# Kernel tuning notes

Measured on AMD Instinct MI355X. Metric: run time of the kernel, lower is better.

The kernel has to match this reference:

```python
import jax, jax.numpy as jnp
import numpy as np

B, S, D, H, DFF = 4, 2048, 768, 12, 3072
DK = D // H

def setup_inputs() -> dict:
    key = jax.random.key(0)
    ks = jax.random.split(key, 16)
    sc = 0.02
    inp = {
        'src': jax.random.normal(ks[0], (B, S, D), jnp.float32),
        'mask': jnp.ones((B, 1, 1, S), jnp.int32),
        'Wq': jax.random.normal(ks[1], (D, D), jnp.float32) * sc,
        'bq': jnp.zeros((D,), jnp.float32),
        'Wk': jax.random.normal(ks[2], (D, D), jnp.float32) * sc,
        'bk': jnp.zeros((D,), jnp.float32),
        'Wv': jax.random.normal(ks[3], (D, D), jnp.float32) * sc,
        'bv': jnp.zeros((D,), jnp.float32),
        'Wo': jax.random.normal(ks[4], (D, D), jnp.float32) * sc,
        'bo': jnp.zeros((D,), jnp.float32),
        'W1': jax.random.normal(ks[5], (D, DFF), jnp.float32) * sc,
        'b1': jnp.zeros((DFF,), jnp.float32),
        'W2': jax.random.normal(ks[6], (DFF, D), jnp.float32) * sc,
        'b2': jnp.zeros((D,), jnp.float32),
        'ln1_g': jnp.ones((D,), jnp.float32), 'ln1_b': jnp.zeros((D,), jnp.float32),
        'ln2_g': jnp.ones((D,), jnp.float32), 'ln2_b': jnp.zeros((D,), jnp.float32),
    }
    return inp

def _layernorm(x, g, b, eps=1e-5):
    mu = jnp.mean(x, axis=-1, keepdims=True)
    var = jnp.mean(jnp.square(x - mu), axis=-1, keepdims=True)
    return (x - mu) * jax.lax.rsqrt(var + eps) * g + b

def reference(src, mask, Wq, bq, Wk, bk, Wv, bv, Wo, bo, W1, b1, W2, b2, ln1_g, ln1_b, ln2_g, ln2_b):
    # Multi-head self-attention (dropout in eval mode -> identity)
    q = (src @ Wq + bq).reshape(B, S, H, DK).transpose(0, 2, 1, 3)  # [B,H,S,dk]
    k = (src @ Wk + bk).reshape(B, S, H, DK).transpose(0, 2, 1, 3)
    v = (src @ Wv + bv).reshape(B, S, H, DK).transpose(0, 2, 1, 3)
    scores = jnp.einsum('bhqd,bhkd->bhqk', q, k) / jnp.sqrt(jnp.float32(DK))
    scores = jnp.where(mask == 0, jnp.float32(-1e9), scores)
    attn = jax.nn.softmax(scores, axis=-1)
    ctx = jnp.einsum('bhqk,bhkd->bhqd', attn, v)  # [B,H,S,dk]
    ctx = ctx.transpose(0, 2, 1, 3).reshape(B, S, D)
    attn_out = ctx @ Wo + bo
    x = _layernorm(src + attn_out, ln1_g, ln1_b)
    ffn = jax.nn.relu(x @ W1 + b1) @ W2 + b2
    return _layernorm(x + ffn, ln2_g, ln2_b)
```

## Files before the change

kernel.cpp:

```cpp
#include <hip/hip_runtime.h>
#include <hip/hip_bf16.h>
#include <stdint.h>

constexpr int BB = 4;
constexpr int SS = 2048;
constexpr int DD = 768;
constexpr int HH = 12;
constexpr int DKK = 64;
constexpr int DFF2 = 3072;
constexpr int MR = BB * SS;

typedef __attribute__((ext_vector_type(4))) short short4v;
typedef __attribute__((ext_vector_type(8))) short short8v;
typedef __attribute__((ext_vector_type(4))) float f32x4;
typedef __attribute__((ext_vector_type(16))) float f32x16;
typedef __attribute__((ext_vector_type(4))) float float4v;
typedef __attribute__((ext_vector_type(4))) unsigned int u32x4;

static __device__ inline short f2bs(float f) {
    __hip_bfloat16 h = __float2bfloat16(f);
    return (short)__builtin_bit_cast(unsigned short, h);
}
static __device__ inline float bs2f(short s) {
    __hip_bfloat16 h = __builtin_bit_cast(__hip_bfloat16, (unsigned short)s);
    return __bfloat162float(h);
}

static __device__ inline void glds16(const void* g, void* l) {
    __builtin_amdgcn_global_load_lds(
        (const __attribute__((address_space(1))) void*)g,
        (__attribute__((address_space(3))) void*)l, 16, 0, 0);
}

static __device__ inline unsigned cvtpk(float a, float b) {
    unsigned d;
    asm("v_cvt_pk_bf16_f32 %0, %1, %2" : "=v"(d) : "v"(a), "v"(b));
    return d;
}
static __device__ inline short8v pk4(unsigned a, unsigned b, unsigned c, unsigned d) {
    u32x4 w; w[0] = a; w[1] = b; w[2] = c; w[3] = d;
    return __builtin_bit_cast(short8v, w);
}

static __device__ inline void bar_vmcnt4() {
    __builtin_amdgcn_sched_barrier(0);
    asm volatile("s_waitcnt vmcnt(4)" ::: "memory");
    __builtin_amdgcn_s_barrier();
    __builtin_amdgcn_sched_barrier(0);
}
static __device__ inline void bar_vmcnt0() {
    __builtin_amdgcn_sched_barrier(0);
    asm volatile("s_waitcnt vmcnt(0)" ::: "memory");
    __builtin_amdgcn_s_barrier();
    __builtin_amdgcn_sched_barrier(0);
}

__global__ __launch_bounds__(256) void cast_f32_bf16(const float* __restrict__ in,
                                                     short* __restrict__ out, int n) {
    int i = (blockIdx.x * 256 + threadIdx.x) * 4;
    if (i < n) {
        float4v v = *(const float4v*)&in[i];
        short4v o;
        o[0] = f2bs(v[0]); o[1] = f2bs(v[1]); o[2] = f2bs(v[2]); o[3] = f2bs(v[3]);
        *(short4v*)&out[i] = o;
    }
}

__global__ __launch_bounds__(256) void transpose_cast(const float* __restrict__ W,
                                                      short* __restrict__ Wt, int K, int N) {
    __shared__ float tile[32][33];
    int n0 = blockIdx.x * 32, k0 = blockIdx.y * 32;
    int tx = threadIdx.x & 31, ty = threadIdx.x >> 5;
    #pragma unroll
    for (int i = 0; i < 32; i += 8)
        tile[ty + i][tx] = W[(size_t)(k0 + ty + i) * N + n0 + tx];
    __syncthreads();
    #pragma unroll
    for (int i = 0; i < 32; i += 8)
        Wt[(size_t)(n0 + ty + i) * K + k0 + tx] = f2bs(tile[tx][ty + i]);
}

__global__ __launch_bounds__(256) void vtrans(const short* __restrict__ V,
                                              short* __restrict__ Vt) {
    __shared__ short t[64][72];
    const int tid = threadIdx.x;
    const size_t base = (size_t)blockIdx.y * SS * DKK;
    const int s0 = blockIdx.x * 64;
    int r = tid >> 3, c = (tid & 7) * 8;
    #pragma unroll
    for (int it = 0; it < 2; it++)
        *(short8v*)&t[it * 32 + r][c] =
            *(const short8v*)&V[base + (size_t)(s0 + it * 32 + r) * DKK + c];
    __syncthreads();
    int d = tid >> 2, grp = (tid & 3) * 16;
    short8v o0, o1;
    #pragma unroll
    for (int e = 0; e < 8; e++) {
        int p0 = e, p1 = 8 + e;
        o0[e] = t[grp + (p0 & 3) + 8 * ((p0 >> 2) & 1) + 4 * (p0 >> 3)][d];
        o1[e] = t[grp + (p1 & 3) + 8 * ((p1 >> 2) & 1) + 4 * (p1 >> 3)][d];
    }
    int c0 = 2 * (tid & 3), c1 = c0 + 1;
    int p0 = c0 ^ (d & 7), p1 = c1 ^ (d & 7);
    *(short8v*)&Vt[base + (size_t)d * SS + s0 + p0 * 8] = o0;
    *(short8v*)&Vt[base + (size_t)d * SS + s0 + p1 * 8] = o1;
}

template <int EPI>
__global__ __launch_bounds__(256) void gemm_bt(
    const short* __restrict__ A, const short* __restrict__ Bt,
    int Nn, int Kn,
    const float* __restrict__ bias0, const float* __restrict__ bias1,
    const float* __restrict__ bias2,
    short* __restrict__ out0, short* __restrict__ out1, short* __restrict__ out2) {
    __shared__ alignas(16) short sA[3][128 * 32];
    __shared__ alignas(16) short sB[3][128 * 32];
    const int tid = threadIdx.x;
    const int wave = tid >> 6, lane = tid & 63;
    const int g = lane >> 4, qq = lane & 15;
    const int wm = (wave >> 1) * 64, wn = (wave & 1) * 64;

    const int gx = gridDim.x;
    const int nwg = gx * gridDim.y;
    const int wgid = blockIdx.y * gx + blockIdx.x;
    const int cpx = nwg >> 3;
    const int swz = (wgid & 7) * cpx + (wgid >> 3);
    const int bx = swz % gx, by = swz / gx;
    const int m0 = by * 128, n0 = bx * 128;

    const int e0 = wave * 512 + lane * 8;
    const int r0 = e0 >> 5, c0 = e0 & 31;

    const f32x4 zero = {0.0f, 0.0f, 0.0f, 0.0f};
    f32x4 acc[4][4];
    #pragma unroll
    for (int i = 0; i < 4; i++)
        #pragma unroll
        for (int j = 0; j < 4; j++) acc[i][j] = zero;

    const int NK = Kn >> 5;
    glds16(&A[(size_t)(m0 + r0) * Kn + c0], &sA[0][wave * 512]);
    glds16(&A[(size_t)(m0 + r0 + 64) * Kn + c0], &sA[0][wave * 512 + 2048]);
    glds16(&Bt[(size_t)(n0 + r0) * Kn + c0], &sB[0][wave * 512]);
    glds16(&Bt[(size_t)(n0 + r0 + 64) * Kn + c0], &sB[0][wave * 512 + 2048]);
    __syncthreads();

    int cur = 0, nxt = 1;
    for (int kt = 0; kt < NK; ++kt) {
        if (kt + 1 < NK) {
            const int k1 = (kt + 1) * 32;
            glds16(&A[(size_t)(m0 + r0) * Kn + k1 + c0], &sA[nxt][wave * 512]);
            glds16(&A[(size_t)(m0 + r0 + 64) * Kn + k1 + c0], &sA[nxt][wave * 512 + 2048]);
            glds16(&Bt[(size_t)(n0 + r0) * Kn + k1 + c0], &sB[nxt][wave * 512]);
            glds16(&Bt[(size_t)(n0 + r0 + 64) * Kn + k1 + c0], &sB[nxt][wave * 512 + 2048]);
            bar_vmcnt4();
        } else {
            bar_vmcnt0();
        }
        short8v af[4], bf[4];
        #pragma unroll
        for (int i = 0; i < 4; i++) {
            af[i] = *(const short8v*)&sA[cur][(wm + i * 16 + qq) * 32 + 8 * g];
            bf[i] = *(const short8v*)&sB[cur][(wn + i * 16 + qq) * 32 + 8 * g];
        }
        #pragma unroll
        for (int i = 0; i < 4; i++)
            #pragma unroll
            for (int j = 0; j < 4; j++)
                acc[i][j] = __builtin_amdgcn_mfma_f32_16x16x32_bf16(af[i], bf[j], acc[i][j], 0, 0, 0);
        cur = nxt;
        nxt = (nxt == 2) ? 0 : nxt + 1;
    }

    if (EPI == 2) {
        int which = bx / 6;
        const float* bias = (which == 0) ? bias0 : ((which == 1) ? bias1 : bias2);
        short* outp = (which == 0) ? out0 : ((which == 1) ? out1 : out2);
        float scale = (which == 0) ? 0.125f * 1.44269504088896f : 1.0f;
        #pragma unroll
        for (int i = 0; i < 4; i++)
            #pragma unroll
            for (int j = 0; j < 4; j++)
                #pragma unroll
                for (int r = 0; r < 4; r++) {
                    int row = m0 + wm + i * 16 + g * 4 + r;
                    int col = n0 - which * DD + wn + j * 16 + qq;
                    float vv = (acc[i][j][r] + bias[col]) * scale;
                    int b_ = row >> 11, s_ = row & 2047;
                    int h_ = col >> 6, d_ = col & 63;
                    if (which == 1)
                        d_ = (((d_ >> 3) ^ (s_ & 7)) << 3) | (d_ & 7);
                    outp[(((size_t)(b_ * HH + h_)) * SS + s_) * DKK + d_] = f2bs(vv);
                }
    } else {
        #pragma unroll
        for (int i = 0; i < 4; i++)
            #pragma unroll
            for (int j = 0; j < 4; j++)
                #pragma unroll
                for (int r = 0; r < 4; r++) {
                    int row = m0 + wm + i * 16 + g * 4 + r;
                    int col = n0 + wn + j * 16 + qq;
                    float vv = acc[i][j][r] + bias0[col];
                    if (EPI == 1) vv = fmaxf(vv, 0.0f);
                    out0[(size_t)row * Nn + col] = f2bs(vv);
                }
    }
}

__global__ __launch_bounds__(256) void attn_kernel(
    const short* __restrict__ Q, const short* __restrict__ Kb,
    const short* __restrict__ Vt, const int* __restrict__ mask,
    short* __restrict__ ctx) {
    __shared__ alignas(16) short sK[3][64 * 64];
    __shared__ alignas(16) short sV[3][64 * 64];
    __shared__ float sAl[4][32];
    __shared__ unsigned char smask[256];
    const int tid = threadIdx.x;
    const int wave = tid >> 6, lane = tid & 63;
    const int hi = lane >> 5, ln = lane & 31;
    constexpr int NT = SS / 64;

    int flat = blockIdx.y * gridDim.x + blockIdx.x;
    int nw = (flat & 7) * 96 + (flat >> 3);
    const int bh = nw >> 4, qb = nw & 15;
    const int b_ = bh / HH, h_ = bh % HH;
    const int q0 = qb * 128 + wave * 32;
    const size_t base = (size_t)bh * SS * DKK;

    {
        const int* mp = mask + b_ * SS + tid * 8;
        unsigned char by = 0;
        #pragma unroll
        for (int e = 0; e < 8; e++) by |= (unsigned char)((mp[e] != 0) << e);
        smask[tid] = by;
    }

    short8v qf[4];
    {
        const short* qp = &Q[base + (size_t)(q0 + ln) * DKK];
        #pragma unroll
        for (int c = 0; c < 4; c++)
            qf[c] = *(const short8v*)(qp + 16 * c + 8 * hi);
    }

    f32x16 O0, O1;
    #pragma unroll
    for (int r = 0; r < 16; r++) { O0[r] = 0.0f; O1[r] = 0.0f; }
    float lreg = 0.0f;

    const int stgrow = wave * 8 + (lane >> 3);
    const int stgc = (lane & 7) * 8;
    const int rsz = (ln & 7) << 4;

    glds16(&Kb[base + (size_t)stgrow * DKK + stgc], &sK[0][wave * 512]);
    glds16(&Kb[base + (size_t)(stgrow + 32) * DKK + stgc], &sK[0][2048 + wave * 512]);
    glds16(&Vt[base + (size_t)stgrow * SS + stgc], &sV[0][wave * 512]);
    glds16(&Vt[base + (size_t)(stgrow + 32) * SS + stgc], &sV[0][2048 + wave * 512]);
    __syncthreads();

    int cur = 0, nxt = 1;
    for (int t = 0; t < NT; ++t) {
        const int kv0 = t * 64;
        if (t + 1 < NT) {
            const int kn = kv0 + 64;
            glds16(&Kb[base + (size_t)(kn + stgrow) * DKK + stgc], &sK[nxt][wave * 512]);
            glds16(&Kb[base + (size_t)(kn + stgrow + 32) * DKK + stgc], &sK[nxt][2048 + wave * 512]);
            glds16(&Vt[base + (size_t)stgrow * SS + kn + stgc], &sV[nxt][wave * 512]);
            glds16(&Vt[base + (size_t)(stgrow + 32) * SS + kn + stgc], &sV[nxt][2048 + wave * 512]);
            bar_vmcnt4();
        } else {
            bar_vmcnt0();
        }
        const char* kr0 = (const char*)&sK[cur][0] + ln * 128;
        const char* kr1 = kr0 + 32 * 128;
        const char* vr0 = (const char*)&sV[cur][0] + ln * 128;
        const char* vr1 = vr0 + 32 * 128;

        f32x16 s0, s1;
        #pragma unroll
        for (int r = 0; r < 16; r++) { s0[r] = 0.0f; s1[r] = 0.0f; }
        __builtin_amdgcn_s_setprio(1);
        #pragma unroll
        for (int c = 0; c < 4; c++) {
            int off = (32 * c + 16 * hi) ^ rsz;
            s0 = __builtin_amdgcn_mfma_f32_32x32x16_bf16(
                *(const short8v*)(kr0 + off), qf[c], s0, 0, 0, 0);
            s1 = __builtin_amdgcn_mfma_f32_32x32x16_bf16(
                *(const short8v*)(kr1 + off), qf[c], s1, 0, 0, 0);
        }
        __builtin_amdgcn_s_setprio(0);

        uint64_t mb = *(const uint64_t*)&smask[kv0 >> 3];
        if (mb != ~0ull) {
            #pragma unroll
            for (int r = 0; r < 16; r++) {
                int kvr = (r & 3) + 8 * (r >> 2) + 4 * hi;
                if (!((mb >> kvr) & 1)) s0[r] = -1.5e9f;
                if (!((mb >> (kvr + 32)) & 1)) s1[r] = -1.5e9f;
            }
        }

        float ps = 0.0f;
        unsigned w0[8], w1[8];
        #pragma unroll
        for (int r8 = 0; r8 < 8; ++r8) {
            float a0 = __builtin_amdgcn_exp2f(s0[2 * r8]);
            float a1 = __builtin_amdgcn_exp2f(s0[2 * r8 + 1]);
            ps += a0 + a1;
            w0[r8] = cvtpk(a0, a1);
            float b0 = __builtin_amdgcn_exp2f(s1[2 * r8]);
            float b1 = __builtin_amdgcn_exp2f(s1[2 * r8 + 1]);
            ps += b0 + b1;
            w1[r8] = cvtpk(b0, b1);
        }
        lreg += ps;

        short8v p00 = pk4(w0[0], w0[1], w0[2], w0[3]);
        short8v p01 = pk4(w0[4], w0[5], w0[6], w0[7]);
        short8v p10 = pk4(w1[0], w1[1], w1[2], w1[3]);
        short8v p11 = pk4(w1[4], w1[5], w1[6], w1[7]);

        __builtin_amdgcn_s_setprio(1);
        #pragma unroll
        for (int cc = 0; cc < 4; cc++) {
            int off = (32 * cc + 16 * hi) ^ rsz;
            short8v pa = (cc == 0) ? p00 : (cc == 1) ? p01 : (cc == 2) ? p10 : p11;
            O0 = __builtin_amdgcn_mfma_f32_32x32x16_bf16(
                pa, *(const short8v*)(vr0 + off), O0, 0, 0, 0);
            O1 = __builtin_amdgcn_mfma_f32_32x32x16_bf16(
                pa, *(const short8v*)(vr1 + off), O1, 0, 0, 0);
        }
        __builtin_amdgcn_s_setprio(0);
        cur = nxt;
        nxt = (nxt == 2) ? 0 : nxt + 1;
    }

    lreg += __shfl_xor(lreg, 32);
    sAl[wave][ln] = 1.0f / lreg;
    #pragma unroll
    for (int r = 0; r < 16; r++) {
        int rho = (r & 3) + 8 * (r >> 2) + 4 * hi;
        float li = sAl[wave][rho];
        size_t rowoff = (size_t)(b_ * SS + q0 + rho) * DD + h_ * DKK;
        ctx[rowoff + ln] = f2bs(O0[r] * li);
        ctx[rowoff + 32 + ln] = f2bs(O1[r] * li);
    }
}

template <int WB, int WF>
__global__ __launch_bounds__(256) void ln_fused(
    const float* __restrict__ in1, const short* __restrict__ in2,
    const float* __restrict__ gw, const float* __restrict__ bw,
    short* __restrict__ outb, float* __restrict__ outf) {
    const int row = blockIdx.x;
    const int tid = threadIdx.x;
    float4v v = {0.0f, 0.0f, 0.0f, 0.0f};
    if (tid < 192) {
        float4v a = *(const float4v*)&in1[(size_t)row * DD + tid * 4];
        short4v b = *(const short4v*)&in2[(size_t)row * DD + tid * 4];
        #pragma unroll
        for (int e = 0; e < 4; e++) v[e] = a[e] + bs2f(b[e]);
    }
    float s = v[0] + v[1] + v[2] + v[3];
    float s2 = v[0] * v[0] + v[1] * v[1] + v[2] * v[2] + v[3] * v[3];
    #pragma unroll
    for (int off = 1; off < 64; off <<= 1) {
        s += __shfl_xor(s, off);
        s2 += __shfl_xor(s2, off);
    }
    __shared__ float red[8];
    int wv = tid >> 6;
    if ((tid & 63) == 0) { red[wv] = s; red[4 + wv] = s2; }
    __syncthreads();
    s = red[0] + red[1] + red[2] + red[3];
    s2 = red[4] + red[5] + red[6] + red[7];
    float mu = s / DD;
    float var = s2 / DD - mu * mu;
    float rs = rsqrtf(var + 1e-5f);
    if (tid < 192) {
        float4v gv = *(const float4v*)&gw[tid * 4];
        float4v bv = *(const float4v*)&bw[tid * 4];
        float4v y;
        #pragma unroll
        for (int e = 0; e < 4; e++) y[e] = (v[e] - mu) * rs * gv[e] + bv[e];
        if (WB) {
            short4v o;
            #pragma unroll
            for (int e = 0; e < 4; e++) o[e] = f2bs(y[e]);
            *(short4v*)&outb[(size_t)row * DD + tid * 4] = o;
        }
        if (WF) *(float4v*)&outf[(size_t)row * DD + tid * 4] = y;
    }
}

extern "C" void kernel_launch(void* const* d_in, const int* in_sizes, int n_in,
                              void* d_out, int out_size, void* d_ws, size_t ws_size,
                              hipStream_t stream) {
    (void)in_sizes; (void)n_in; (void)out_size; (void)ws_size;
    const float* src = (const float*)d_in[0];
    const int* mask = (const int*)d_in[1];
    const float* Wq = (const float*)d_in[2];
    const float* bq = (const float*)d_in[3];
    const float* Wk = (const float*)d_in[4];
    const float* bk = (const float*)d_in[5];
    const float* Wv = (const float*)d_in[6];
    const float* bv = (const float*)d_in[7];
    const float* Wo = (const float*)d_in[8];
    const float* bo = (const float*)d_in[9];
    const float* W1 = (const float*)d_in[10];
    const float* b1 = (const float*)d_in[11];
    const float* W2 = (const float*)d_in[12];
    const float* b2 = (const float*)d_in[13];
    const float* ln1_g = (const float*)d_in[14];
    const float* ln1_b = (const float*)d_in[15];
    const float* ln2_g = (const float*)d_in[16];
    const float* ln2_b = (const float*)d_in[17];

    char* ws = (char*)d_ws;
    const size_t SB = (size_t)MR * DD * 2;
    short* src_b  = (short*)(ws);
    short* Wqkv_t = (short*)(ws + SB);
    short* qb     = (short*)(ws + SB + 3538944);
    short* kb_    = qb + (size_t)MR * DD;
    short* vb_    = kb_ + (size_t)MR * DD;
    short* ctxb   = vb_ + (size_t)MR * DD;
    short* hb     = qb;
    short* Wo_t   = (short*)(ws + SB + 3538944 + 4 * SB);
    short* x_b    = (short*)(ws + SB + 3538944 + 4 * SB + 1179648);
    short* W1_t   = (short*)((char*)x_b + SB);
    short* W2_t   = (short*)((char*)W1_t + 4718592);
    float* x_f    = (float*)((char*)W2_t + 4718592);
    short* vt_    = x_b;
    short* attn_b = src_b;
    short* ffn_b  = src_b;

    cast_f32_bf16<<<(MR * DD) / 1024, 256, 0, stream>>>(src, src_b, MR * DD);
    transpose_cast<<<dim3(24, 24), 256, 0, stream>>>(Wq, Wqkv_t, DD, DD);
    transpose_cast<<<dim3(24, 24), 256, 0, stream>>>(Wk, Wqkv_t + DD * DD, DD, DD);
    transpose_cast<<<dim3(24, 24), 256, 0, stream>>>(Wv, Wqkv_t + 2 * DD * DD, DD, DD);
    transpose_cast<<<dim3(24, 24), 256, 0, stream>>>(Wo, Wo_t, DD, DD);
    transpose_cast<<<dim3(96, 24), 256, 0, stream>>>(W1, W1_t, DD, DFF2);
    transpose_cast<<<dim3(24, 96), 256, 0, stream>>>(W2, W2_t, DFF2, DD);

    gemm_bt<2><<<dim3(2304 / 128, MR / 128), 256, 0, stream>>>(
        src_b, Wqkv_t, 2304, DD, bq, bk, bv, qb, kb_, vb_);

    vtrans<<<dim3(SS / 64, BB * HH), 256, 0, stream>>>(vb_, vt_);

    attn_kernel<<<dim3(SS / 128, BB * HH), 256, 0, stream>>>(qb, kb_, vt_, mask, ctxb);

    gemm_bt<0><<<dim3(DD / 128, MR / 128), 256, 0, stream>>>(
        ctxb, Wo_t, DD, DD, bo, nullptr, nullptr, attn_b, nullptr, nullptr);

    ln_fused<1, 1><<<MR, 256, 0, stream>>>(src, attn_b, ln1_g, ln1_b, x_b, x_f);

    gemm_bt<1><<<dim3(DFF2 / 128, MR / 128), 256, 0, stream>>>(
        x_b, W1_t, DFF2, DD, b1, nullptr, nullptr, hb, nullptr, nullptr);
    gemm_bt<0><<<dim3(DD / 128, MR / 128), 256, 0, stream>>>(
        hb, W2_t, DD, DFF2, b2, nullptr, nullptr, ffn_b, nullptr, nullptr);

    ln_fused<0, 1><<<MR, 256, 0, stream>>>(x_f, ffn_b, ln2_g, ln2_b, nullptr, (float*)d_out);
}
```

Before: 318.0 us.

## Compute softmax row sums via MFMA and drop fp32 residual copy

```diff
diff --git a/kernel.cpp b/kernel.cpp
--- a/kernel.cpp
+++ b/kernel.cpp
@@ -214,7 +214,6 @@
     short* __restrict__ ctx) {
     __shared__ alignas(16) short sK[3][64 * 64];
     __shared__ alignas(16) short sV[3][64 * 64];
-    __shared__ float sAl[4][32];
     __shared__ unsigned char smask[256];
     const int tid = threadIdx.x;
     const int wave = tid >> 6, lane = tid & 63;
@@ -244,10 +243,15 @@
             qf[c] = *(const short8v*)(qp + 16 * c + 8 * hi);
     }
 
-    f32x16 O0, O1;
-    #pragma unroll
-    for (int r = 0; r < 16; r++) { O0[r] = 0.0f; O1[r] = 0.0f; }
-    float lreg = 0.0f;
+    f32x16 O0, O1, Lacc;
+    #pragma unroll
+    for (int r = 0; r < 16; r++) { O0[r] = 0.0f; O1[r] = 0.0f; Lacc[r] = 0.0f; }
+    f32x16 ZEROV;
+    #pragma unroll
+    for (int r = 0; r < 16; r++) ZEROV[r] = 0.0f;
+    short8v ones8;
+    #pragma unroll
+    for (int e = 0; e < 8; e++) ones8[e] = (short)0x3F80;
 
     const int stgrow = wave * 8 + (lane >> 3);
     const int stgc = (lane & 7) * 8;
@@ -278,11 +282,16 @@
         const char* vr1 = vr0 + 32 * 128;
 
         f32x16 s0, s1;
-        #pragma unroll
-        for (int r = 0; r < 16; r++) { s0[r] = 0.0f; s1[r] = 0.0f; }
         __builtin_amdgcn_s_setprio(1);
-        #pragma unroll
-        for (int c = 0; c < 4; c++) {
+        {
+            int off = (16 * hi) ^ rsz;
+            s0 = __builtin_amdgcn_mfma_f32_32x32x16_bf16(
+                *(const short8v*)(kr0 + off), qf[0], ZEROV, 0, 0, 0);
+            s1 = __builtin_amdgcn_mfma_f32_32x32x16_bf16(
+                *(const short8v*)(kr1 + off), qf[0], ZEROV, 0, 0, 0);
+        }
+        #pragma unroll
+        for (int c = 1; c < 4; c++) {
             int off = (32 * c + 16 * hi) ^ rsz;
             s0 = __builtin_amdgcn_mfma_f32_32x32x16_bf16(
                 *(const short8v*)(kr0 + off), qf[c], s0, 0, 0, 0);
@@ -301,20 +310,16 @@
             }
         }
 
-        float ps = 0.0f;
         unsigned w0[8], w1[8];
         #pragma unroll
         for (int r8 = 0; r8 < 8; ++r8) {
             float a0 = __builtin_amdgcn_exp2f(s0[2 * r8]);
             float a1 = __builtin_amdgcn_exp2f(s0[2 * r8 + 1]);
-            ps += a0 + a1;
             w0[r8] = cvtpk(a0, a1);
             float b0 = __builtin_amdgcn_exp2f(s1[2 * r8]);
             float b1 = __builtin_amdgcn_exp2f(s1[2 * r8 + 1]);
-            ps += b0 + b1;
             w1[r8] = cvtpk(b0, b1);
         }
-        lreg += ps;
 
         short8v p00 = pk4(w0[0], w0[1], w0[2], w0[3]);
         short8v p01 = pk4(w0[4], w0[5], w0[6], w0[7]);
@@ -330,37 +335,42 @@
                 pa, *(const short8v*)(vr0 + off), O0, 0, 0, 0);
             O1 = __builtin_amdgcn_mfma_f32_32x32x16_bf16(
                 pa, *(const short8v*)(vr1 + off), O1, 0, 0, 0);
+            Lacc = __builtin_amdgcn_mfma_f32_32x32x16_bf16(pa, ones8, Lacc, 0, 0, 0);
         }
         __builtin_amdgcn_s_setprio(0);
         cur = nxt;
         nxt = (nxt == 2) ? 0 : nxt + 1;
     }
 
-    lreg += __shfl_xor(lreg, 32);
-    sAl[wave][ln] = 1.0f / lreg;
     #pragma unroll
     for (int r = 0; r < 16; r++) {
         int rho = (r & 3) + 8 * (r >> 2) + 4 * hi;
-        float li = sAl[wave][rho];
+        float li = 1.0f / Lacc[r];
         size_t rowoff = (size_t)(b_ * SS + q0 + rho) * DD + h_ * DKK;
         ctx[rowoff + ln] = f2bs(O0[r] * li);
         ctx[rowoff + 32 + ln] = f2bs(O1[r] * li);
     }
 }
 
-template <int WB, int WF>
+template <int IN1BF, int WB, int WF>
 __global__ __launch_bounds__(256) void ln_fused(
-    const float* __restrict__ in1, const short* __restrict__ in2,
+    const void* __restrict__ in1v, const short* __restrict__ in2,
     const float* __restrict__ gw, const float* __restrict__ bw,
     short* __restrict__ outb, float* __restrict__ outf) {
     const int row = blockIdx.x;
     const int tid = threadIdx.x;
     float4v v = {0.0f, 0.0f, 0.0f, 0.0f};
     if (tid < 192) {
-        float4v a = *(const float4v*)&in1[(size_t)row * DD + tid * 4];
         short4v b = *(const short4v*)&in2[(size_t)row * DD + tid * 4];
-        #pragma unroll
-        for (int e = 0; e < 4; e++) v[e] = a[e] + bs2f(b[e]);
+        if (IN1BF) {
+            short4v a = *(const short4v*)&((const short*)in1v)[(size_t)row * DD + tid * 4];
+            #pragma unroll
+            for (int e = 0; e < 4; e++) v[e] = bs2f(a[e]) + bs2f(b[e]);
+        } else {
+            float4v a = *(const float4v*)&((const float*)in1v)[(size_t)row * DD + tid * 4];
+            #pragma unroll
+            for (int e = 0; e < 4; e++) v[e] = a[e] + bs2f(b[e]);
+        }
     }
     float s = v[0] + v[1] + v[2] + v[3];
     float s2 = v[0] * v[0] + v[1] * v[1] + v[2] * v[2] + v[3] * v[3];
@@ -430,7 +440,6 @@
     short* x_b    = (short*)(ws + SB + 3538944 + 4 * SB + 1179648);
     short* W1_t   = (short*)((char*)x_b + SB);
     short* W2_t   = (short*)((char*)W1_t + 4718592);
-    float* x_f    = (float*)((char*)W2_t + 4718592);
     short* vt_    = x_b;
     short* attn_b = src_b;
     short* ffn_b  = src_b;
@@ -453,12 +462,12 @@
     gemm_bt<0><<<dim3(DD / 128, MR / 128), 256, 0, stream>>>(
         ctxb, Wo_t, DD, DD, bo, nullptr, nullptr, attn_b, nullptr, nullptr);
 
-    ln_fused<1, 1><<<MR, 256, 0, stream>>>(src, attn_b, ln1_g, ln1_b, x_b, x_f);
+    ln_fused<0, 1, 0><<<MR, 256, 0, stream>>>(src, attn_b, ln1_g, ln1_b, x_b, nullptr);
 
     gemm_bt<1><<<dim3(DFF2 / 128, MR / 128), 256, 0, stream>>>(
         x_b, W1_t, DFF2, DD, b1, nullptr, nullptr, hb, nullptr, nullptr);
     gemm_bt<0><<<dim3(DD / 128, MR / 128), 256, 0, stream>>>(
         hb, W2_t, DD, DFF2, b2, nullptr, nullptr, ffn_b, nullptr, nullptr);
 
-    ln_fused<0, 1><<<MR, 256, 0, stream>>>(x_f, ffn_b, ln2_g, ln2_b, nullptr, (float*)d_out);
-}
+    ln_fused<1, 0, 1><<<MR, 256, 0, stream>>>(x_b, ffn_b, ln2_g, ln2_b, nullptr, (float*)d_out);
+}
```

After: 316.3 us. No clear change (-0.6%).
